# Optimization experiments

Hardware: AMD Instinct MI355X
Metric: run time of the kernel (lower is better)

The kernel has to match this reference:

```python
import jax, jax.numpy as jnp
import numpy as np

N, DIM, T_ITERS = 8192, 64, 4

def setup_inputs() -> dict:
    key = jax.random.key(0)
    ks = jax.random.split(key, 9)
    graph = jax.random.normal(ks[0], (N, N), jnp.float32)
    x = jax.random.randint(ks[1], (N,), 0, 2, jnp.int32)  # 0/1 indicator of S
    theta1 = jax.random.normal(ks[2], (1, DIM), jnp.float32)
    theta2 = jax.random.normal(ks[3], (DIM, DIM), jnp.float32)
    theta3 = jax.random.normal(ks[4], (DIM, DIM), jnp.float32)
    theta4 = jax.random.normal(ks[5], (1, DIM), jnp.float32)
    theta5 = jax.random.normal(ks[6], (2 * DIM, 1), jnp.float32)
    theta6 = jax.random.normal(ks[7], (DIM, DIM), jnp.float32)
    theta7 = jax.random.normal(ks[8], (DIM, DIM), jnp.float32)
    return dict(graph=graph, x=x, theta1=theta1, theta2=theta2, theta3=theta3,
                theta4=theta4, theta5=theta5, theta6=theta6, theta7=theta7,
                v=100, T=T_ITERS)


def reference(graph, x, theta1, theta2, theta3, theta4, theta5, theta6, theta7, v, T):
    dt = graph.dtype
    xf = x.astype(dt)  # (N,)
    # c_v = sum_u relu(theta4 * graph[v,u]) @ theta3.
    # Exact identity: relu(t*w) = max(w,0)*relu(t) + max(-w,0)*relu(-t),
    s_pos = jnp.maximum(graph, 0.0).sum(axis=1)   # (N,)
    s_neg = jnp.maximum(-graph, 0.0).sum(axis=1)  # (N,)
    t4 = theta4[0]  # (dim,)
    c = (s_pos[:, None] * jax.nn.relu(t4)
         + s_neg[:, None] * jax.nn.relu(-t4)) @ theta3  # (N, dim)
    a = xf[:, None] * theta1  # (N, dim) via broadcast of (1, dim)

    def step(u, _):
        summ = u.sum(axis=0, keepdims=True)        # (1, dim)
        b = (summ - u) @ theta2                    # (N, dim)
        return jax.nn.relu(a + b + c), None

    u0 = jnp.zeros((graph.shape[0], theta1.shape[1]), dt)
    u, _ = jax.lax.scan(step, u0, None, length=T)

    summ = u.sum(axis=0)                           # (dim,)
    q_in = jnp.concatenate([summ @ theta6, u[v] @ theta7])  # (2*dim,)
    return jax.nn.relu(q_in) @ theta5              # (1,)
```

## Files before the change

kernel.cpp:

```cpp
#include <hip/hip_runtime.h>

#define NN 8192
#define DIM 64
#define T_IT 4
#define NPART 8

typedef float nfloat4 __attribute__((ext_vector_type(4)));

__global__ void prep_kernel(const float* __restrict__ theta3,
                            const float* __restrict__ theta4,
                            float* __restrict__ pq,
                            float* __restrict__ summ1_parts,
                            float* __restrict__ summ) {
  const int d = threadIdx.x;
  float p = 0.f, q = 0.f;
  for (int k = 0; k < DIM; ++k) {
    const float t4 = theta4[k];
    const float th = theta3[k * DIM + d];
    p += fmaxf(t4, 0.f) * th;
    q += fmaxf(-t4, 0.f) * th;
  }
  pq[d] = p;
  pq[DIM + d] = q;
#pragma unroll
  for (int c = 0; c < NPART; ++c) summ1_parts[c * DIM + d] = 0.f;
#pragma unroll
  for (int t = 0; t < T_IT - 1; ++t) summ[t * DIM + d] = 0.f;
}

__global__ __launch_bounds__(256) void fused_rowsum_step1(
    const float* __restrict__ graph, const int* __restrict__ x,
    const float* __restrict__ theta1, const float* __restrict__ pq,
    float* __restrict__ s_pos, float* __restrict__ s_neg,
    float* __restrict__ u, float* __restrict__ summ1_parts) {
  const int wave = threadIdx.x >> 6;
  const int lane = threadIdx.x & 63;
  const int row = blockIdx.x * 4 + wave;
  const float pd = pq[lane];
  const float qd = pq[DIM + lane];
  const float t1d = theta1[lane];

  const nfloat4* g = (const nfloat4*)(graph + (size_t)row * NN);
  float sp = 0.f, sn = 0.f;
  for (int it = 0; it < NN / 4 / 64; it += 8) {
#pragma unroll
    for (int j = 0; j < 8; ++j) {
      const nfloat4 v = __builtin_nontemporal_load(&g[lane + (it + j) * 64]);
      sp += fmaxf(v.x, 0.f) + fmaxf(v.y, 0.f) + fmaxf(v.z, 0.f) + fmaxf(v.w, 0.f);
      sn += fmaxf(-v.x, 0.f) + fmaxf(-v.y, 0.f) + fmaxf(-v.z, 0.f) + fmaxf(-v.w, 0.f);
    }
  }
#pragma unroll
  for (int off = 32; off > 0; off >>= 1) {
    sp += __shfl_down(sp, off);
    sn += __shfl_down(sn, off);
  }
  sp = __shfl(sp, 0);
  sn = __shfl(sn, 0);
  if (lane == 0) {
    s_pos[row] = sp;
    s_neg[row] = sn;
  }
  const float uv = fmaxf((float)x[row] * t1d + sp * pd + sn * qd, 0.f);
  u[(size_t)row * DIM + lane] = uv;

  __shared__ float red[4][DIM];
  red[wave][lane] = uv;
  __syncthreads();
  if (wave == 0)
    atomicAdd(&summ1_parts[(blockIdx.x & (NPART - 1)) * DIM + lane],
              red[0][lane] + red[1][lane] + red[2][lane] + red[3][lane]);
}

__global__ __launch_bounds__(256) void step_kernel(
    const float* __restrict__ theta1, const float* __restrict__ theta2,
    const int* __restrict__ x, const float* __restrict__ s_pos,
    const float* __restrict__ s_neg, const float* __restrict__ pq,
    const float* __restrict__ summ_in, int ncopies,
    float* __restrict__ summ_out, float* __restrict__ u) {
  __shared__ float th2[DIM * DIM];
  __shared__ float sin_sh[DIM];
  __shared__ float gsh[DIM];
  __shared__ __align__(16) float ush[4][DIM];
  __shared__ float red[4][DIM];
  const int t = threadIdx.x;
  const int d = t & 63;
  const int r = t >> 6;

  for (int i = t; i < DIM * DIM; i += 256) th2[i] = theta2[i];
  if (t < DIM) {
    float s = 0.f;
    for (int c = 0; c < ncopies; ++c) s += summ_in[c * DIM + t];
    sin_sh[t] = s;
  }
  __syncthreads();
  if (t < DIM) {
    float g = 0.f;
    for (int k = 0; k < DIM; ++k) g += sin_sh[k] * th2[k * DIM + d];
    gsh[d] = g;
  }
  const float pd = pq[d];
  const float qd = pq[DIM + d];
  const float t1d = theta1[d];
  __syncthreads();
  const float gd = gsh[d];

  float acc = 0.f;
  for (int base = blockIdx.x * 4; base < NN; base += gridDim.x * 4) {
    const int row = base + r;
    ush[r][d] = u[(size_t)row * DIM + d];
    __syncthreads();
    float dot = 0.f;
    const float4* ur = (const float4*)ush[r];
#pragma unroll
    for (int kk = 0; kk < DIM / 4; ++kk) {
      const float4 uv = ur[kk];
      dot += uv.x * th2[(4 * kk + 0) * DIM + d];
      dot += uv.y * th2[(4 * kk + 1) * DIM + d];
      dot += uv.z * th2[(4 * kk + 2) * DIM + d];
      dot += uv.w * th2[(4 * kk + 3) * DIM + d];
    }
    const float acv = (float)x[row] * t1d + s_pos[row] * pd + s_neg[row] * qd;
    float val = fmaxf(acv + gd - dot, 0.f);
    u[(size_t)row * DIM + d] = val;
    acc += val;
    __syncthreads();
  }
  red[r][d] = acc;
  __syncthreads();
  if (r == 0) {
    atomicAdd(&summ_out[d], red[0][d] + red[1][d] + red[2][d] + red[3][d]);
  }
}

__global__ void final_kernel(const float* __restrict__ theta5,
                             const float* __restrict__ theta6,
                             const float* __restrict__ theta7,
                             const float* __restrict__ summ,
                             const float* __restrict__ u,
                             const int* __restrict__ vptr,
                             float* __restrict__ out) {
  const int t = threadIdx.x;
  const int d = t & 63;
  float h;
  if (t < DIM) {
    float s = 0.f;
    for (int k = 0; k < DIM; ++k) s += summ[k] * theta6[k * DIM + d];
    h = fmaxf(s, 0.f) * theta5[d];
  } else {
    const int v = *vptr;
    const float* uv = u + (size_t)v * DIM;
    float s = 0.f;
    for (int k = 0; k < DIM; ++k) s += uv[k] * theta7[k * DIM + d];
    h = fmaxf(s, 0.f) * theta5[DIM + d];
  }
  __shared__ float red[128];
  red[t] = h;
  __syncthreads();
  if (t == 0) {
    float s = 0.f;
    for (int i = 0; i < 128; ++i) s += red[i];
    out[0] = s;
  }
}

extern "C" void kernel_launch(void* const* d_in, const int* in_sizes, int n_in,
                              void* d_out, int out_size, void* d_ws, size_t ws_size,
                              hipStream_t stream) {
  const float* graph  = (const float*)d_in[0];
  const int*   x      = (const int*)d_in[1];
  const float* theta1 = (const float*)d_in[2];
  const float* theta2 = (const float*)d_in[3];
  const float* theta3 = (const float*)d_in[4];
  const float* theta4 = (const float*)d_in[5];
  const float* theta5 = (const float*)d_in[6];
  const float* theta6 = (const float*)d_in[7];
  const float* theta7 = (const float*)d_in[8];
  const int*   vptr   = (const int*)d_in[9];
  float* out = (float*)d_out;

  float* ws     = (float*)d_ws;
  float* pq     = ws;
  float* parts  = ws + 128;
  float* summ   = ws + 128 + NPART * DIM;
  float* s_pos  = summ + (T_IT - 1) * DIM;
  float* s_neg  = s_pos + NN;
  float* u      = s_neg + NN;

  prep_kernel<<<1, DIM, 0, stream>>>(theta3, theta4, pq, parts, summ);
  fused_rowsum_step1<<<2048, 256, 0, stream>>>(graph, x, theta1, pq,
                                               s_pos, s_neg, u, parts);
  step_kernel<<<256, 256, 0, stream>>>(theta1, theta2, x, s_pos, s_neg, pq,
                                       parts, NPART, summ + 0 * DIM, u);
  for (int t = 2; t < T_IT; ++t) {
    step_kernel<<<256, 256, 0, stream>>>(theta1, theta2, x, s_pos, s_neg, pq,
                                         summ + (t - 2) * DIM, 1,
                                         summ + (t - 1) * DIM, u);
  }
  final_kernel<<<1, 128, 0, stream>>>(theta5, theta6, theta7,
                                      summ + (T_IT - 2) * DIM, u, vptr, out);
}
```

Before: 410.5 us.

## Fuse step iterations and final head into one cooperative persistent kernel

Moves the recurrent step iterations and the final readout into a single cooperative kernel with 256 blocks that each keep 32 rows of u in shared memory and theta2 columns in registers, using grid.sync between iterations. This removes several kernel launches and the global round trips of u between steps. The graph row-sum kernel is slimmed to only produce s_pos/s_neg and zero the sum buffer. It adds grid-wide barrier cost and high register pressure from the 64-float theta2 cache, and relies on cooperative launch residency.

```diff
diff --git a/kernel.cpp b/kernel.cpp
--- a/kernel.cpp
+++ b/kernel.cpp
@@ -1,44 +1,25 @@
 #include <hip/hip_runtime.h>
+#include <hip/hip_cooperative_groups.h>
+
+namespace cg = cooperative_groups;
 
 #define NN 8192
 #define DIM 64
 #define T_IT 4
-#define NPART 8
+#define NBLK_STEPS 256
+#define ROWS_PER_BLK (NN / NBLK_STEPS)
 
 typedef float nfloat4 __attribute__((ext_vector_type(4)));
 
-__global__ void prep_kernel(const float* __restrict__ theta3,
-                            const float* __restrict__ theta4,
-                            float* __restrict__ pq,
-                            float* __restrict__ summ1_parts,
-                            float* __restrict__ summ) {
-  const int d = threadIdx.x;
-  float p = 0.f, q = 0.f;
-  for (int k = 0; k < DIM; ++k) {
-    const float t4 = theta4[k];
-    const float th = theta3[k * DIM + d];
-    p += fmaxf(t4, 0.f) * th;
-    q += fmaxf(-t4, 0.f) * th;
-  }
-  pq[d] = p;
-  pq[DIM + d] = q;
-#pragma unroll
-  for (int c = 0; c < NPART; ++c) summ1_parts[c * DIM + d] = 0.f;
-#pragma unroll
-  for (int t = 0; t < T_IT - 1; ++t) summ[t * DIM + d] = 0.f;
-}
+__global__ __launch_bounds__(256) void rowsum_kernel(
+    const float* __restrict__ graph,
+    float* __restrict__ s_pos, float* __restrict__ s_neg,
+    float* __restrict__ summ_g ) {
+  if (blockIdx.x == 0) summ_g[threadIdx.x] = 0.f;
 
-__global__ __launch_bounds__(256) void fused_rowsum_step1(
-    const float* __restrict__ graph, const int* __restrict__ x,
-    const float* __restrict__ theta1, const float* __restrict__ pq,
-    float* __restrict__ s_pos, float* __restrict__ s_neg,
-    float* __restrict__ u, float* __restrict__ summ1_parts) {
   const int wave = threadIdx.x >> 6;
   const int lane = threadIdx.x & 63;
   const int row = blockIdx.x * 4 + wave;
-  const float pd = pq[lane];
-  const float qd = pq[DIM + lane];
-  const float t1d = theta1[lane];
 
   const nfloat4* g = (const nfloat4*)(graph + (size_t)row * NN);
   float sp = 0.f, sn = 0.f;
@@ -55,118 +36,131 @@
     sp += __shfl_down(sp, off);
     sn += __shfl_down(sn, off);
   }
-  sp = __shfl(sp, 0);
-  sn = __shfl(sn, 0);
   if (lane == 0) {
     s_pos[row] = sp;
     s_neg[row] = sn;
   }
-  const float uv = fmaxf((float)x[row] * t1d + sp * pd + sn * qd, 0.f);
-  u[(size_t)row * DIM + lane] = uv;
-
-  __shared__ float red[4][DIM];
-  red[wave][lane] = uv;
-  __syncthreads();
-  if (wave == 0)
-    atomicAdd(&summ1_parts[(blockIdx.x & (NPART - 1)) * DIM + lane],
-              red[0][lane] + red[1][lane] + red[2][lane] + red[3][lane]);
 }
 
-__global__ __launch_bounds__(256) void step_kernel(
+__global__ __launch_bounds__(256, 1) void steps_kernel(
     const float* __restrict__ theta1, const float* __restrict__ theta2,
-    const int* __restrict__ x, const float* __restrict__ s_pos,
-    const float* __restrict__ s_neg, const float* __restrict__ pq,
-    const float* __restrict__ summ_in, int ncopies,
-    float* __restrict__ summ_out, float* __restrict__ u) {
-  __shared__ float th2[DIM * DIM];
-  __shared__ float sin_sh[DIM];
-  __shared__ float gsh[DIM];
-  __shared__ __align__(16) float ush[4][DIM];
+    const float* __restrict__ theta3, const float* __restrict__ theta4,
+    const float* __restrict__ theta5, const float* __restrict__ theta6,
+    const float* __restrict__ theta7, const int* __restrict__ x,
+    const float* __restrict__ s_pos, const float* __restrict__ s_neg,
+    const int* __restrict__ vptr, float* __restrict__ summ_g,
+    float* __restrict__ out) {
+  __shared__ __align__(16) float ub[ROWS_PER_BLK][DIM];
   __shared__ float red[4][DIM];
+  __shared__ float ssh[DIM];
   const int t = threadIdx.x;
   const int d = t & 63;
-  const int r = t >> 6;
+  const int rg = t >> 6;
+  const int row0 = blockIdx.x * ROWS_PER_BLK;
 
-  for (int i = t; i < DIM * DIM; i += 256) th2[i] = theta2[i];
-  if (t < DIM) {
-    float s = 0.f;
-    for (int c = 0; c < ncopies; ++c) s += summ_in[c * DIM + t];
-    sin_sh[t] = s;
+  float t2c[DIM];
+#pragma unroll
+  for (int k = 0; k < DIM; ++k) t2c[k] = theta2[k * DIM + d];
+
+  float pd = 0.f, qd = 0.f;
+#pragma unroll 8
+  for (int k = 0; k < DIM; ++k) {
+    const float t4 = theta4[k];
+    const float th = theta3[k * DIM + d];
+    pd += fmaxf(t4, 0.f) * th;
+    qd += fmaxf(-t4, 0.f) * th;
   }
+  const float t1d = theta1[d];
+
+  float acv[8];
+#pragma unroll
+  for (int j = 0; j < 8; ++j) {
+    const int row = row0 + rg * 8 + j;
+    acv[j] = (float)x[row] * t1d + s_pos[row] * pd + s_neg[row] * qd;
+  }
+
+  cg::grid_group grid = cg::this_grid();
+
+  float part = 0.f;
+#pragma unroll
+  for (int j = 0; j < 8; ++j) {
+    const float v = fmaxf(acv[j], 0.f);
+    ub[rg * 8 + j][d] = v;
+    part += v;
+  }
+  red[rg][d] = part;
   __syncthreads();
-  if (t < DIM) {
-    float g = 0.f;
-    for (int k = 0; k < DIM; ++k) g += sin_sh[k] * th2[k * DIM + d];
-    gsh[d] = g;
+  if (rg == 0)
+    atomicAdd(&summ_g[0 * DIM + d],
+              red[0][d] + red[1][d] + red[2][d] + red[3][d]);
+
+  for (int st = 1; st < T_IT; ++st) {
+    __threadfence();
+    grid.sync();
+    if (t < DIM) ssh[t] = summ_g[(st - 1) * DIM + t];
+    __syncthreads();
+    float gd = 0.f;
+#pragma unroll
+    for (int k = 0; k < DIM; ++k) gd += ssh[k] * t2c[k];
+    float vals[8];
+#pragma unroll
+    for (int j = 0; j < 8; ++j) {
+      const float4* ur = (const float4*)&ub[rg * 8 + j][0];
+      float dot = 0.f;
+#pragma unroll
+      for (int kk = 0; kk < DIM / 4; ++kk) {
+        const float4 uv = ur[kk];
+        dot += uv.x * t2c[4 * kk + 0] + uv.y * t2c[4 * kk + 1] +
+               uv.z * t2c[4 * kk + 2] + uv.w * t2c[4 * kk + 3];
+      }
+      vals[j] = fmaxf(acv[j] + gd - dot, 0.f);
+    }
+    __syncthreads();
+    part = 0.f;
+#pragma unroll
+    for (int j = 0; j < 8; ++j) {
+      ub[rg * 8 + j][d] = vals[j];
+      part += vals[j];
+    }
+    red[rg][d] = part;
+    __syncthreads();
+    if (rg == 0)
+      atomicAdd(&summ_g[st * DIM + d],
+                red[0][d] + red[1][d] + red[2][d] + red[3][d]);
   }
-  const float pd = pq[d];
-  const float qd = pq[DIM + d];
-  const float t1d = theta1[d];
-  __syncthreads();
-  const float gd = gsh[d];
+  __threadfence();
+  grid.sync();
 
-  float acc = 0.f;
-  for (int base = blockIdx.x * 4; base < NN; base += gridDim.x * 4) {
-    const int row = base + r;
-    ush[r][d] = u[(size_t)row * DIM + d];
+  const int v = *vptr;
+  if (blockIdx.x == (v >> 5)) {
+    float h = 0.f;
+    if (t < DIM) {
+      float s = 0.f;
+#pragma unroll 8
+      for (int k = 0; k < DIM; ++k)
+        s += summ_g[(T_IT - 1) * DIM + k] * theta6[k * DIM + t];
+      h = fmaxf(s, 0.f) * theta5[t];
+    } else if (t < 2 * DIM) {
+      const int vr = v & (ROWS_PER_BLK - 1);
+      float s = 0.f;
+#pragma unroll 8
+      for (int k = 0; k < DIM; ++k) s += ub[vr][k] * theta7[k * DIM + d];
+      h = fmaxf(s, 0.f) * theta5[DIM + d];
+    }
     __syncthreads();
-    float dot = 0.f;
-    const float4* ur = (const float4*)ush[r];
-#pragma unroll
-    for (int kk = 0; kk < DIM / 4; ++kk) {
-      const float4 uv = ur[kk];
-      dot += uv.x * th2[(4 * kk + 0) * DIM + d];
-      dot += uv.y * th2[(4 * kk + 1) * DIM + d];
-      dot += uv.z * th2[(4 * kk + 2) * DIM + d];
-      dot += uv.w * th2[(4 * kk + 3) * DIM + d];
+    ((float*)red)[t] = h;
+    __syncthreads();
+    if (t == 0) {
+      float s = 0.f;
+      for (int i = 0; i < 2 * DIM; ++i) s += ((float*)red)[i];
+      out[0] = s;
     }
-    const float acv = (float)x[row] * t1d + s_pos[row] * pd + s_neg[row] * qd;
-    float val = fmaxf(acv + gd - dot, 0.f);
-    u[(size_t)row * DIM + d] = val;
-    acc += val;
-    __syncthreads();
-  }
-  red[r][d] = acc;
-  __syncthreads();
-  if (r == 0) {
-    atomicAdd(&summ_out[d], red[0][d] + red[1][d] + red[2][d] + red[3][d]);
-  }
-}
-
-__global__ void final_kernel(const float* __restrict__ theta5,
-                             const float* __restrict__ theta6,
-                             const float* __restrict__ theta7,
-                             const float* __restrict__ summ,
-                             const float* __restrict__ u,
-                             const int* __restrict__ vptr,
-                             float* __restrict__ out) {
-  const int t = threadIdx.x;
-  const int d = t & 63;
-  float h;
-  if (t < DIM) {
-    float s = 0.f;
-    for (int k = 0; k < DIM; ++k) s += summ[k] * theta6[k * DIM + d];
-    h = fmaxf(s, 0.f) * theta5[d];
-  } else {
-    const int v = *vptr;
-    const float* uv = u + (size_t)v * DIM;
-    float s = 0.f;
-    for (int k = 0; k < DIM; ++k) s += uv[k] * theta7[k * DIM + d];
-    h = fmaxf(s, 0.f) * theta5[DIM + d];
-  }
-  __shared__ float red[128];
-  red[t] = h;
-  __syncthreads();
-  if (t == 0) {
-    float s = 0.f;
-    for (int i = 0; i < 128; ++i) s += red[i];
-    out[0] = s;
   }
 }
 
 extern "C" void kernel_launch(void* const* d_in, const int* in_sizes, int n_in,
-                              void* d_out, int out_size, void* d_ws, size_t ws_size,
-                              hipStream_t stream) {
+                              void* d_out, int out_size, void* d_ws,
+                              size_t ws_size, hipStream_t stream) {
   const float* graph  = (const float*)d_in[0];
   const int*   x      = (const int*)d_in[1];
   const float* theta1 = (const float*)d_in[2];
@@ -179,24 +173,18 @@
   const int*   vptr   = (const int*)d_in[9];
   float* out = (float*)d_out;
 
-  float* ws     = (float*)d_ws;
-  float* pq     = ws;
-  float* parts  = ws + 128;
-  float* summ   = ws + 128 + NPART * DIM;
-  float* s_pos  = summ + (T_IT - 1) * DIM;
-  float* s_neg  = s_pos + NN;
-  float* u      = s_neg + NN;
+  float* ws    = (float*)d_ws;
+  float* s_pos = ws;
+  float* s_neg = ws + NN;
+  float* summ  = ws + 2 * NN;
 
-  prep_kernel<<<1, DIM, 0, stream>>>(theta3, theta4, pq, parts, summ);
-  fused_rowsum_step1<<<2048, 256, 0, stream>>>(graph, x, theta1, pq,
-                                               s_pos, s_neg, u, parts);
-  step_kernel<<<256, 256, 0, stream>>>(theta1, theta2, x, s_pos, s_neg, pq,
-                                       parts, NPART, summ + 0 * DIM, u);
-  for (int t = 2; t < T_IT; ++t) {
-    step_kernel<<<256, 256, 0, stream>>>(theta1, theta2, x, s_pos, s_neg, pq,
-                                         summ + (t - 2) * DIM, 1,
-                                         summ + (t - 1) * DIM, u);
-  }
-  final_kernel<<<1, 128, 0, stream>>>(theta5, theta6, theta7,
-                                      summ + (T_IT - 2) * DIM, u, vptr, out);
+  rowsum_kernel<<<2048, 256, 0, stream>>>(graph, s_pos, s_neg, summ);
+
+  void* args[] = {(void*)&theta1, (void*)&theta2, (void*)&theta3,
+                  (void*)&theta4, (void*)&theta5, (void*)&theta6,
+                  (void*)&theta7, (void*)&x,      (void*)&s_pos,
+                  (void*)&s_neg,  (void*)&vptr,   (void*)&summ,
+                  (void*)&out};
+  hipLaunchCooperativeKernel(reinterpret_cast<void*>(steps_kernel),
+                             dim3(NBLK_STEPS), dim3(256), args, 0, stream);
 }
```

New measurement: 587.7 us. 1.43x slower.
